# Performance work log

Hardware: AMD Instinct MI355X
Metric: run time of the kernel (lower is better)

The kernel has to match this reference:

```python
import jax, jax.numpy as jnp
import numpy as np

H = 1024          # hidden_size
NH = 16           # num_heads = hidden_size // head_dim
DK = 64           # head_dim (key)
DV = 64           # head_v_dim
VDIM = 1024       # value_dim
DECAY_LR, GATE_LR, A_LR, V_LR = 64, 160, 64, 64
W_SCALE = -0.6065306597126334  # -exp(-0.5)
GN_EPS = 64 * 1e-5             # head_dim * norm_eps


def _lora(x, A, B, b, act):
    h = x @ A.T
    if act is not None:
        h = act(h)
    y = h @ B.T
    return y if b is None else y + b


def setup_inputs() -> dict:
    key = jax.random.key(0)
    ks = iter(jax.random.split(key, 40))
    def n(shape, s=0.02):
        return jax.random.normal(next(ks), shape, dtype=jnp.float32) * s
    inp = {
        'hidden_states': jax.random.normal(next(ks), (8, 2048, H), jnp.float32),
        'v_first': jax.random.normal(next(ks), (8, 2048, VDIM), jnp.float32),
        'x_r': n((1, 1, H), 0.5), 'x_w': n((1, 1, H), 0.5), 'x_k': n((1, 1, H), 0.5),
        'x_v': n((1, 1, H), 0.5), 'x_a': n((1, 1, H), 0.5), 'x_g': n((1, 1, H), 0.5),
        'k_k': 0.71 + n((H,), 0.05),
        'k_a': 1.02 + n((H,), 0.05),
        'r_k': -0.04 + n((NH, DK), 0.05),
        'W_r': n((H, H)), 'W_k': n((H, H)), 'W_v': n((VDIM, H)), 'W_o': n((H, VDIM)),
        'w_lora_A': n((DECAY_LR, H)), 'w_lora_B': n((H, DECAY_LR)), 'w_lora_b': n((H,), 0.5) - 4.0,
        'a_lora_A': n((A_LR, H)), 'a_lora_B': n((H, A_LR)), 'a_lora_b': n((H,), 0.1),
        'v_lora_A': n((V_LR, H)), 'v_lora_B': n((VDIM, V_LR)), 'v_lora_b': 0.73 + n((VDIM,), 0.1),
        'g_lora_A': n((GATE_LR, H)), 'g_lora_B': n((VDIM, GATE_LR)),
        'gn_w': jnp.ones((VDIM,), jnp.float32), 'gn_b': jnp.zeros((VDIM,), jnp.float32),
    }
    return inp


def reference(hidden_states, v_first, x_r, x_w, x_k, x_v, x_a, x_g, k_k, k_a, r_k,
              W_r, W_k, W_v, W_o, w_lora_A, w_lora_B, w_lora_b,
              a_lora_A, a_lora_B, a_lora_b, v_lora_A, v_lora_B, v_lora_b,
              g_lora_A, g_lora_B, gn_w, gn_b):
    x = hidden_states
    B_, T, _ = x.shape
    # token shift: delta[t] = x[t-1] - x[t], x[-1] = 0
    shifted = jnp.pad(x, ((0, 0), (1, 0), (0, 0)))[:, :T]
    delta = shifted - x
    xr = x + delta * x_r; xw = x + delta * x_w; xk = x + delta * x_k
    xv = x + delta * x_v; xa = x + delta * x_a; xg = x + delta * x_g

    r = xr @ W_r.T
    w = W_SCALE * jax.nn.sigmoid(_lora(xw, w_lora_A, w_lora_B, w_lora_b, jnp.tanh))  # log-decay in (-e^-0.5, 0)
    k = xk @ W_k.T
    v = xv @ W_v.T
    v = v + (v_first - v) * jax.nn.sigmoid(_lora(xv, v_lora_A, v_lora_B, v_lora_b, None))  # layer_idx != 0
    a = jax.nn.sigmoid(_lora(xa, a_lora_A, a_lora_B, a_lora_b, None))
    g = _lora(xg, g_lora_A, g_lora_B, None, jax.nn.sigmoid)

    kk = (k * k_k).reshape(B_, T, NH, DK)
    kk = kk / jnp.maximum(jnp.linalg.norm(kk, axis=-1, keepdims=True), 1e-12)  # l2 norm per head
    k = k * (1.0 + (a - 1.0) * k_a)

    rh = r.reshape(B_, T, NH, DK)
    wh = w.reshape(B_, T, NH, DK)
    kh = k.reshape(B_, T, NH, DK)
    vh = v.reshape(B_, T, NH, DV)
    ah = -kk                               # delta-rule 'a' (removal direction)
    bh = kk * a.reshape(B_, T, NH, DK)     # delta-rule 'b' (write direction)

    def step(S, inputs):
        # S: [B, H, DK, DV]; inputs each [B, H, D]
        r_t, w_t, k_t, v_t, a_t, b_t = inputs
        sa = jnp.einsum('bhk,bhkv->bhv', a_t, S)
        S = S * jnp.exp(w_t)[..., None] \
            + jnp.einsum('bhk,bhv->bhkv', b_t, sa) \
            + jnp.einsum('bhk,bhv->bhkv', k_t, v_t)
        o_t = jnp.einsum('bhk,bhkv->bhv', r_t, S)
        return S, o_t

    seq = tuple(jnp.moveaxis(t, 1, 0) for t in (rh, wh, kh, vh, ah, bh))  # [T,B,H,D]
    S0 = jnp.zeros((B_, NH, DK, DV), dtype=x.dtype)
    _, o = jax.lax.scan(step, S0, seq)
    o = jnp.moveaxis(o, 0, 1)  # [B, T, NH, DV]

    # GroupNorm with num_groups = num_heads over value_dim channels == per-head LayerNorm (no per-head affine)
    mu = o.mean(-1, keepdims=True)
    var = o.var(-1, keepdims=True)
    on = ((o - mu) / jnp.sqrt(var + GN_EPS)).reshape(B_, T, VDIM) * gn_w + gn_b

    bonus = ((rh * kh * r_k).sum(-1, keepdims=True) * vh).reshape(B_, T, VDIM)
    out = ((on + bonus) * g) @ W_o.T
    return out
```

## Files before the change

### kernel.cpp

```cpp
#include <hip/hip_runtime.h>
#include <hip/hip_bf16.h>


#define DEVI __device__ __forceinline__

constexpr int TSEQ = 2048;
constexpr int HID  = 1024;
constexpr int BTOT = 16384;
constexpr int CCH  = 32;
constexpr int NCH  = TSEQ / CCH;
constexpr int L4N  = 352;
constexpr float W_SCALE = -0.6065306597126334f;
constexpr float GN_EPS  = 6.4e-4f;

using s16x8  = __attribute__((ext_vector_type(8))) short;
using f32x4v = __attribute__((ext_vector_type(4))) float;

DEVI float4 ld4(const float* p) { return *reinterpret_cast<const float4*>(p); }
DEVI void   st4(float* p, float4 v) { *reinterpret_cast<float4*>(p) = v; }
DEVI float  sigf(float x) { return 1.0f / (1.0f + __expf(-x)); }
DEVI unsigned short bfr(float f) {
    unsigned int u = __float_as_uint(f);
    return (unsigned short)((u + 0x7fffu + ((u >> 16) & 1u)) >> 16);
}
DEVI float bff(unsigned short s) { return __uint_as_float(((unsigned int)s) << 16); }
DEVI unsigned int pk2(float lo, float hi) {
    return ((unsigned int)bfr(hi) << 16) | (unsigned int)bfr(lo);
}
DEVI f32x4v MF(s16x8 a, s16x8 b, f32x4v c) {
    return __builtin_amdgcn_mfma_f32_16x16x32_bf16(a, b, c, 0, 0, 0);
}
DEVI void gl16(const void* g, void* l) {
    __builtin_amdgcn_global_load_lds(
        (const __attribute__((address_space(1))) unsigned int*)g,
        (__attribute__((address_space(3))) unsigned int*)l, 16, 0, 0);
}
DEVI void gl4(const void* g, void* l) {
    __builtin_amdgcn_global_load_lds(
        (const __attribute__((address_space(1))) unsigned int*)g,
        (__attribute__((address_space(3))) unsigned int*)l, 4, 0, 0);
}

__global__ __launch_bounds__(256) void cast_kernel(
        const float* __restrict__ s, unsigned short* __restrict__ d, int n) {
    int i = (blockIdx.x * 256 + threadIdx.x) * 4;
    if (i >= n) return;
    float4 v = ld4(s + i);
    ushort4 o; o.x = bfr(v.x); o.y = bfr(v.y); o.z = bfr(v.z); o.w = bfr(v.w);
    *reinterpret_cast<ushort4*>(d + i) = o;
}

__global__ __launch_bounds__(256) void proj3_kernel(
        const float* __restrict__ x,
        const float* __restrict__ cr, const float* __restrict__ ck,
        const float* __restrict__ cv,
        const unsigned short* __restrict__ Wr, const unsigned short* __restrict__ Wk,
        const unsigned short* __restrict__ Wv,
        unsigned short* __restrict__ Ro, unsigned short* __restrict__ Ko,
        unsigned short* __restrict__ Vo) {
    __shared__ __align__(16) unsigned short As[3][64 * 32];
    __shared__ __align__(16) unsigned short Bs[3][128 * 32];
    const int tid = threadIdx.x;
    const int w = tid >> 6, l = tid & 63;
    const int bm = blockIdx.x * 64, bn = blockIdx.y * 128;
    const int wm = w >> 1, wn = w & 1;
    const int lr = l & 15, lq = l >> 4, lk = lq * 8;

    f32x4v acc[3][2][4];
#pragma unroll
    for (int p = 0; p < 3; p++)
#pragma unroll
        for (int i = 0; i < 2; i++)
#pragma unroll
            for (int j = 0; j < 4; j++)
#pragma unroll
                for (int q = 0; q < 4; q++) acc[p][i][j][q] = 0.f;

    const float* cvs[3] = {cr, ck, cv};
    const unsigned short* Ws[3] = {Wr, Wk, Wv};

    for (int k0 = 0; k0 < HID; k0 += 32) {
        {
            const int row = tid >> 2, kp = (tid & 3) * 8;
            const int gr = bm + row;
            const float* xp = x + (size_t)gr * HID + k0 + kp;
            float4 x0 = ld4(xp), x1 = ld4(xp + 4);
            float4 p0 = make_float4(0.f, 0.f, 0.f, 0.f), p1 = p0;
            if ((gr & (TSEQ - 1)) != 0) { p0 = ld4(xp - HID); p1 = ld4(xp - HID + 4); }
            float xb[8] = {x0.x, x0.y, x0.z, x0.w, x1.x, x1.y, x1.z, x1.w};
            float dx[8] = {p0.x - x0.x, p0.y - x0.y, p0.z - x0.z, p0.w - x0.w,
                           p1.x - x1.x, p1.y - x1.y, p1.z - x1.z, p1.w - x1.w};
#pragma unroll
            for (int p = 0; p < 3; p++) {
                float4 c0 = ld4(cvs[p] + k0 + kp), c1 = ld4(cvs[p] + k0 + kp + 4);
                float cc[8] = {c0.x, c0.y, c0.z, c0.w, c1.x, c1.y, c1.z, c1.w};
                uint4 u;
                u.x = pk2(fmaf(dx[0], cc[0], xb[0]), fmaf(dx[1], cc[1], xb[1]));
                u.y = pk2(fmaf(dx[2], cc[2], xb[2]), fmaf(dx[3], cc[3], xb[3]));
                u.z = pk2(fmaf(dx[4], cc[4], xb[4]), fmaf(dx[5], cc[5], xb[5]));
                u.w = pk2(fmaf(dx[6], cc[6], xb[6]), fmaf(dx[7], cc[7], xb[7]));
                *reinterpret_cast<uint4*>(&As[p][row * 32 + kp]) = u;
            }
        }
#pragma unroll
        for (int p = 0; p < 3; p++)
#pragma unroll
            for (int c = 0; c < 2; c++) {
                int idx = c * 256 + tid;
                int rw = idx >> 2, kp2 = (idx & 3) * 8;
                gl16(Ws[p] + (size_t)(bn + rw) * HID + k0 + kp2,
                     &Bs[p][c * 2048 + w * 512]);
            }
        __syncthreads();
#pragma unroll
        for (int p = 0; p < 3; p++) {
            s16x8 af[2], bf4[4];
#pragma unroll
            for (int i = 0; i < 2; i++)
                af[i] = *reinterpret_cast<const s16x8*>(
                    &As[p][(wm * 32 + i * 16 + lr) * 32 + lk]);
#pragma unroll
            for (int j = 0; j < 4; j++)
                bf4[j] = *reinterpret_cast<const s16x8*>(
                    &Bs[p][(wn * 64 + j * 16 + lr) * 32 + lk]);
#pragma unroll
            for (int i = 0; i < 2; i++)
#pragma unroll
                for (int j = 0; j < 4; j++)
                    acc[p][i][j] = MF(af[i], bf4[j], acc[p][i][j]);
        }
        __syncthreads();
    }

    unsigned short* dsts[3] = {Ro, Ko, Vo};
#pragma unroll
    for (int p = 0; p < 3; p++)
#pragma unroll
        for (int i = 0; i < 2; i++)
#pragma unroll
            for (int j = 0; j < 4; j++)
#pragma unroll
                for (int q = 0; q < 4; q++) {
                    const int grow = bm + wm * 32 + i * 16 + lq * 4 + q;
                    const int gcol = bn + wn * 64 + j * 16 + lr;
                    dsts[p][(size_t)grow * HID + gcol] = bfr(acc[p][i][j][q]);
                }
}

__global__ __launch_bounds__(256) void lora4_kernel(
        const float* __restrict__ x,
        const float* __restrict__ cv_, const float* __restrict__ cw_,
        const float* __restrict__ ca_, const float* __restrict__ cg_,
        const unsigned short* __restrict__ LW, unsigned short* __restrict__ H1) {
    __shared__ __align__(16) unsigned short As[4][64 * 32];
    __shared__ __align__(16) unsigned short Bs[L4N * 32];
    const int tid = threadIdx.x;
    const int w = tid >> 6, l = tid & 63;
    const int lr = l & 15, lq = l >> 4, lk = lq * 8;
    const int bm = blockIdx.x * 64;
    const float* cvs[4] = {cv_, cw_, ca_, cg_};

    f32x4v acc[22];
#pragma unroll
    for (int j = 0; j < 22; j++)
#pragma unroll
        for (int q = 0; q < 4; q++) acc[j][q] = 0.f;

    for (int k0 = 0; k0 < HID; k0 += 32) {
        {
            const int row = tid >> 2, kp = (tid & 3) * 8;
            const int gr = bm + row;
            const float* xp = x + (size_t)gr * HID + k0 + kp;
            float4 x0 = ld4(xp), x1 = ld4(xp + 4);
            float4 p0 = make_float4(0.f, 0.f, 0.f, 0.f), p1 = p0;
            if ((gr & (TSEQ - 1)) != 0) { p0 = ld4(xp - HID); p1 = ld4(xp - HID + 4); }
            float xb[8] = {x0.x, x0.y, x0.z, x0.w, x1.x, x1.y, x1.z, x1.w};
            float dx[8] = {p0.x - x0.x, p0.y - x0.y, p0.z - x0.z, p0.w - x0.w,
                           p1.x - x1.x, p1.y - x1.y, p1.z - x1.z, p1.w - x1.w};
#pragma unroll
            for (int p = 0; p < 4; p++) {
                float4 c0 = ld4(cvs[p] + k0 + kp), c1 = ld4(cvs[p] + k0 + kp + 4);
                float cc[8] = {c0.x, c0.y, c0.z, c0.w, c1.x, c1.y, c1.z, c1.w};
                uint4 u;
                u.x = pk2(fmaf(dx[0], cc[0], xb[0]), fmaf(dx[1], cc[1], xb[1]));
                u.y = pk2(fmaf(dx[2], cc[2], xb[2]), fmaf(dx[3], cc[3], xb[3]));
                u.z = pk2(fmaf(dx[4], cc[4], xb[4]), fmaf(dx[5], cc[5], xb[5]));
                u.w = pk2(fmaf(dx[6], cc[6], xb[6]), fmaf(dx[7], cc[7], xb[7]));
                *reinterpret_cast<uint4*>(&As[p][row * 32 + kp]) = u;
            }
        }
#pragma unroll
        for (int c = 0; c < 6; c++) {
            int idx = c * 256 + tid;
            if (idx < L4N * 4) {
                gl16(LW + (size_t)(idx >> 2) * HID + (idx & 3) * 8 + k0,
                     (char*)&Bs[0] + (c * 256 + w * 64) * 16);
            }
        }
        __syncthreads();
        s16x8 af[4];
#pragma unroll
        for (int p = 0; p < 4; p++)
            af[p] = *reinterpret_cast<const s16x8*>(&As[p][(w * 16 + lr) * 32 + lk]);
#pragma unroll
        for (int j = 0; j < 22; j++) {
            const int grp = (j < 4) ? 0 : (j < 8) ? 1 : (j < 12) ? 2 : 3;
            s16x8 bf = *reinterpret_cast<const s16x8*>(&Bs[(j * 16 + lr) * 32 + lk]);
            acc[j] = MF(af[grp], bf, acc[j]);
        }
        __syncthreads();
    }

#pragma unroll
    for (int j = 0; j < 22; j++)
#pragma unroll
        for (int q = 0; q < 4; q++) {
            const int grow = bm + w * 16 + lq * 4 + q;
            const int gcol = j * 16 + lr;
            float d = acc[j][q];
            if (j >= 4 && j < 8) d = tanhf(d);
            else if (j >= 12) d = sigf(d);
            H1[(size_t)grow * L4N + gcol] = bfr(d);
        }
}

template<int BM, int BN, int MODE, bool OUTBF>
__global__ __launch_bounds__(256) void mgemm(
        const unsigned short* __restrict__ Ab, const unsigned short* __restrict__ Bw,
        void* Cout, int N, int K, int lda,
        const float* __restrict__ bias,
        const unsigned short* aux1, const float* __restrict__ aux2) {
    constexpr int BK = 32;
    constexpr int WM_ = (BN == 128) ? 2 : 4;
    constexpr int WN_ = (BN == 128) ? 2 : 1;
    constexpr int WTM = BM / WM_, WTN = BN / WN_;
    constexpr int MF_ = WTM / 16, NF = WTN / 16;
    constexpr int ACALLS = (BM * BK) / 2048;
    constexpr int BCALLS = (BN * BK) / 2048;
    __shared__ __align__(16) unsigned short As[BM * BK];
    __shared__ __align__(16) unsigned short Bs[BN * BK];
    const int tid = threadIdx.x;
    const int w = tid >> 6, l = tid & 63;
    const int bm = blockIdx.x * BM, bn = blockIdx.y * BN;
    const int wm = w / WN_, wn = w % WN_;
    const int lr = l & 15, lk = (l >> 4) * 8;

    f32x4v acc[MF_][NF];
#pragma unroll
    for (int i = 0; i < MF_; i++)
#pragma unroll
        for (int j = 0; j < NF; j++)
#pragma unroll
            for (int q = 0; q < 4; q++) acc[i][j][q] = 0.f;

    for (int k0 = 0; k0 < K; k0 += BK) {
#pragma unroll
        for (int c = 0; c < ACALLS; c++) {
            int idx = c * 256 + tid;
            int row = idx >> 2, kp = (idx & 3) * 8;
            gl16(Ab + (size_t)(bm + row) * lda + k0 + kp, &As[c * 2048 + w * 512]);
        }
#pragma unroll
        for (int c = 0; c < BCALLS; c++) {
            int idx = c * 256 + tid;
            int row = idx >> 2, kp = (idx & 3) * 8;
            int gc = bn + row; if (gc > N - 1) gc = N - 1;
            gl16(Bw + (size_t)gc * K + k0 + kp, &Bs[c * 2048 + w * 512]);
        }
        __syncthreads();
        s16x8 afx[MF_], bfx[NF];
#pragma unroll
        for (int i = 0; i < MF_; i++)
            afx[i] = *reinterpret_cast<const s16x8*>(&As[(wm * WTM + i * 16 + lr) * BK + lk]);
#pragma unroll
        for (int j = 0; j < NF; j++)
            bfx[j] = *reinterpret_cast<const s16x8*>(&Bs[(wn * WTN + j * 16 + lr) * BK + lk]);
#pragma unroll
        for (int i = 0; i < MF_; i++)
#pragma unroll
            for (int j = 0; j < NF; j++)
                acc[i][j] = __builtin_amdgcn_mfma_f32_16x16x32_bf16(
                    afx[i], bfx[j], acc[i][j], 0, 0, 0);
        __syncthreads();
    }

#pragma unroll
    for (int i = 0; i < MF_; i++) {
        const int grow0 = bm + wm * WTM + i * 16 + (l >> 4) * 4;
#pragma unroll
        for (int j = 0; j < NF; j++) {
            const int gcol = bn + wn * WTN + j * 16 + lr;
            if (gcol >= N) continue;
            const float bsv = (MODE >= 4) ? bias[gcol] : 0.f;
#pragma unroll
            for (int q = 0; q < 4; q++) {
                const int grow = grow0 + q;
                float d = acc[i][j][q];
                if (MODE == 4) d = sigf(d + bsv);
                else if (MODE == 5) {
                    float v0 = bff(aux1[(size_t)grow * N + gcol]);
                    d = fmaf(aux2[(size_t)grow * N + gcol] - v0, sigf(d + bsv), v0);
                }
                else if (MODE == 6) d = W_SCALE * sigf(d + bsv);
                if (OUTBF) ((unsigned short*)Cout)[(size_t)grow * N + gcol] = bfr(d);
                else       ((float*)Cout)[(size_t)grow * N + gcol] = d;
            }
        }
    }
}

__global__ __launch_bounds__(64) void cprep_kernel(
        unsigned short* __restrict__ K16, unsigned short* __restrict__ A16,
        unsigned short* __restrict__ R16, unsigned short* __restrict__ KK16,
        const unsigned short* __restrict__ W16,
        const float* __restrict__ kkc, const float* __restrict__ kac,
        const float* __restrict__ rkw,
        float* __restrict__ SB, float* __restrict__ Ed,
        unsigned short* __restrict__ MvH, unsigned short* __restrict__ MvL) {
    __shared__ __align__(16) unsigned short sA[32][64], sB[32][64];
    __shared__ __align__(16) float Mab[32][36];
    const int bid = blockIdx.x;
    const int bh = bid >> 6, ch = bid & 63;
    const int bb = bh >> 4, hh = bh & 15;
    const int l = threadIdx.x;
    const int chn = hh * 64 + l;
    const float kkcv = kkc[chn], kacv = kac[chn], rkv = rkw[chn];
    size_t off = ((size_t)(bb * TSEQ) + ch * CCH) * HID + chn;
    float cw = 0.f, er = 1.f;
    for (int i = 0; i < CCH; i++, off += HID) {
        const float k = bff(K16[off]);
        const float a = bff(A16[off]);
        const float r = bff(R16[off]);
        const float wv = bff(W16[off]);
        const float kr = k * kkcv;
        float ss = kr * kr;
        ss += __shfl_xor(ss, 1);  ss += __shfl_xor(ss, 2);
        ss += __shfl_xor(ss, 4);  ss += __shfl_xor(ss, 8);
        ss += __shfl_xor(ss, 16); ss += __shfl_xor(ss, 32);
        const float inv = 1.0f / fmaxf(sqrtf(ss), 1e-12f);
        const float kk = kr * inv;
        const float b  = kk * a;
        const float kn = k * fmaf(a - 1.0f, kacv, 1.0f);
        float s3 = r * kn * rkv;
        s3 += __shfl_xor(s3, 1);  s3 += __shfl_xor(s3, 2);
        s3 += __shfl_xor(s3, 4);  s3 += __shfl_xor(s3, 8);
        s3 += __shfl_xor(s3, 16); s3 += __shfl_xor(s3, 32);
        if (l == 0) SB[(size_t)bh * TSEQ + ch * CCH + i] = s3;
        const float cwp = cw; cw += wv;
        const float ea = __expf(cwp), ei = __expf(-cw);
        er = __expf(cw);
        const unsigned short At = bfr(-kk * ea);
        const unsigned short Bt = bfr(b * ei);
        KK16[off] = At;
        A16[off]  = Bt;
        K16[off]  = bfr(kn * ei);
        R16[off]  = bfr(r * er);
        sA[i][l] = At; sB[i][l] = Bt;
    }
    Ed[((size_t)bh * NCH + ch) * 64 + l] = er;
    __syncthreads();
    const int lr = l & 15, lq = l >> 4;
    f32x4v z4; z4[0] = z4[1] = z4[2] = z4[3] = 0.f;
#pragma unroll
    for (int mi = 0; mi < 2; mi++)
#pragma unroll
        for (int ni = 0; ni < 2; ni++) {
            s16x8 a0 = *reinterpret_cast<const s16x8*>(&sA[mi * 16 + lr][lq * 8]);
            s16x8 a1 = *reinterpret_cast<const s16x8*>(&sA[mi * 16 + lr][32 + lq * 8]);
            s16x8 b0 = *reinterpret_cast<const s16x8*>(&sB[ni * 16 + lr][lq * 8]);
            s16x8 b1 = *reinterpret_cast<const s16x8*>(&sB[ni * 16 + lr][32 + lq * 8]);
            f32x4v m = MF(a1, b1, MF(a0, b0, z4));
#pragma unroll
            for (int q = 0; q < 4; q++) {
                int r = mi * 16 + lq * 4 + q, cc2 = ni * 16 + lr;
                Mab[r][cc2] = (cc2 < r) ? m[q] : 0.f;
            }
        }
    __syncthreads();
    const int j = l & 31;
    float m[32];
#pragma unroll
    for (int i = 0; i < 32; i++) m[i] = (i == j) ? 1.f : 0.f;
#pragma unroll
    for (int i = 1; i < 32; i++) {
        float p0 = 0.f, p1 = 0.f, p2 = 0.f, p3 = 0.f;
#pragma unroll
        for (int k4_ = 0; k4_ < 32; k4_ += 4) {
            if (k4_ >= i) break;
            float4 L4 = *reinterpret_cast<const float4*>(&Mab[i][k4_]);
            p0 = fmaf(L4.x, m[k4_ + 0], p0);
            if (k4_ + 1 < i) p1 = fmaf(L4.y, m[k4_ + 1], p1);
            if (k4_ + 2 < i) p2 = fmaf(L4.z, m[k4_ + 2], p2);
            if (k4_ + 3 < i) p3 = fmaf(L4.w, m[k4_ + 3], p3);
        }
        m[i] += (p0 + p1) + (p2 + p3);
    }
    if (l < 32) {
        unsigned short* dH = MvH + (size_t)(bh * NCH + ch) * 1024;
        unsigned short* dL = MvL + (size_t)(bh * NCH + ch) * 1024;
#pragma unroll
        for (int i = 0; i < 32; i++) {
            unsigned short h = bfr(m[i]);
            dH[i * 32 + j] = h;
            dL[i * 32 + j] = bfr(m[i] - bff(h));
        }
    }
}

__global__ __launch_bounds__(256) void recchunk_kernel(
        const unsigned short* __restrict__ AtG, const unsigned short* __restrict__ BtG,
        const unsigned short* __restrict__ KtG, const unsigned short* __restrict__ RtG,
        const unsigned short* __restrict__ V16, const float* __restrict__ Ed,
        const unsigned short* __restrict__ MvH, const unsigned short* __restrict__ MvL,
        float* __restrict__ Ob) {
    __shared__ __align__(16) unsigned short stT[2][4][CCH][64];
    __shared__ __align__(16) unsigned short stMh[2][32][32], stMl[2][32][32];
    __shared__ __align__(16) unsigned short stV[2][CCH][16];
    __shared__ __align__(16) float stEd[2][64];
    __shared__ __align__(16) unsigned short Shi[16][74], Slo[16][74];
    __shared__ __align__(16) unsigned short BtT[64][42], KtT[64][42];
    __shared__ __align__(16) unsigned short VT[16][42];
    __shared__ __align__(16) unsigned short MakH[32][42], MakL[32][42];
    __shared__ __align__(16) unsigned short MrkH[32][42], MrkL[32][42];
    __shared__ __align__(16) unsigned short MrbH[32][42], MrbL[32][42];
    __shared__ __align__(16) unsigned short rhTH[16][42], rhTL[16][42];

    const int bid = blockIdx.x;
    const int vq = bid >> 7, bh = bid & 127;
    const int tid = threadIdx.x;
    const int w = tid >> 6, l = tid & 63;
    const int lr = l & 15, lq = l >> 4;
    const int bb = bh >> 4, hh = bh & 15;
    const size_t rowoff = ((size_t)bb * TSEQ) * HID + hh * 64;
    const int mi = w >> 1, ni = w & 1;

    const int r8 = l >> 3, ck = l & 7;
    const int swz8 = (ck ^ r8) * 8;

    auto STAGE = [&](int buf, int cn) {
        if (cn >= NCH) return;
        const size_t cb = rowoff + (size_t)(cn * CCH) * HID;
        const unsigned short* srcs[4] = {AtG, BtG, KtG, RtG};
        const unsigned short* T = srcs[w];
#pragma unroll
        for (int c = 0; c < 4; c++)
            gl16(T + cb + (size_t)(c * 8 + r8) * HID + swz8, &stT[buf][w][c * 8][0]);
        if (w == 0) {
            gl16(V16 + cb + (size_t)(l >> 1) * HID + vq * 16 + (l & 1) * 8,
                 &stV[buf][0][0]);
            gl4(Ed + ((size_t)bh * NCH + cn) * 64 + l, &stEd[buf][0]);
        } else if (w == 1) {
#pragma unroll
            for (int c = 0; c < 2; c++)
                gl16(MvH + (size_t)(bh * NCH + cn) * 1024 + c * 512 + l * 8,
                     (char*)&stMh[buf][0][0] + c * 1024);
        } else if (w == 2) {
#pragma unroll
            for (int c = 0; c < 2; c++)
                gl16(MvL + (size_t)(bh * NCH + cn) * 1024 + c * 512 + l * 8,
                     (char*)&stMl[buf][0][0] + c * 1024);
        }
    };

    for (int idx = tid; idx < 16 * 74; idx += 256) {
        ((unsigned short*)Shi)[idx] = 0;
        ((unsigned short*)Slo)[idx] = 0;
    }
    STAGE(0, 0);
    asm volatile("s_waitcnt vmcnt(0)" ::: "memory");
    __syncthreads();

    auto fragT = [&](int bf, int tn, int rbase, int kb) -> s16x8 {
        int row = rbase + lr;
        int chv = ((kb >> 3) + lq) ^ (row & 7);
        return *reinterpret_cast<const s16x8*>(
            (const char*)&stT[bf][tn][0][0] + row * 128 + chv * 16);
    };
    auto fragS = [&](const unsigned short (*Sx)[74], int kb) -> s16x8 {
        return *reinterpret_cast<const s16x8*>(&Sx[lr][kb + lq * 8]);
    };
    auto frag42 = [&](const unsigned short (*T)[42], int rbase) -> s16x8 {
        return *reinterpret_cast<const s16x8*>(&T[rbase + lr][lq * 8]);
    };

    f32x4v Sacc;
#pragma unroll
    for (int q = 0; q < 4; q++) Sacc[q] = 0.f;
    f32x4v z4; z4[0] = z4[1] = z4[2] = z4[3] = 0.f;

    int buf = 0;
    for (int c = 0; c < NCH; c++) {
        STAGE(buf ^ 1, c + 1);
        {
            const int tt = tid & 31, g8 = tid >> 5;
            const int ch = g8 ^ (tt & 7);
            uint4 bu = *reinterpret_cast<const uint4*>(&stT[buf][1][tt][ch * 8]);
            uint4 ku = *reinterpret_cast<const uint4*>(&stT[buf][2][tt][ch * 8]);
            unsigned int bw[4] = {bu.x, bu.y, bu.z, bu.w};
            unsigned int kw[4] = {ku.x, ku.y, ku.z, ku.w};
#pragma unroll
            for (int e = 0; e < 4; e++) {
                BtT[g8 * 8 + 2 * e][tt]     = (unsigned short)(bw[e] & 0xffffu);
                BtT[g8 * 8 + 2 * e + 1][tt] = (unsigned short)(bw[e] >> 16);
                KtT[g8 * 8 + 2 * e][tt]     = (unsigned short)(kw[e] & 0xffffu);
                KtT[g8 * 8 + 2 * e + 1][tt] = (unsigned short)(kw[e] >> 16);
            }
            if (g8 < 4) {
                ushort4 vu = *reinterpret_cast<const ushort4*>(&stV[buf][tt][g8 * 4]);
                VT[g8 * 4 + 0][tt] = vu.x; VT[g8 * 4 + 1][tt] = vu.y;
                VT[g8 * 4 + 2][tt] = vu.z; VT[g8 * 4 + 3][tt] = vu.w;
            }
        }
        s16x8 atm0 = fragT(buf, 0, mi * 16, 0), atm1 = fragT(buf, 0, mi * 16, 32);
        s16x8 rt0  = fragT(buf, 3, mi * 16, 0), rt1  = fragT(buf, 3, mi * 16, 32);
        s16x8 bt0  = fragT(buf, 1, ni * 16, 0), bt1  = fragT(buf, 1, ni * 16, 32);
        s16x8 kt0  = fragT(buf, 2, ni * 16, 0), kt1  = fragT(buf, 2, ni * 16, 32);
        f32x4v mak = MF(atm1, kt1, MF(atm0, kt0, z4));
        f32x4v mrk = MF(rt1, kt1, MF(rt0, kt0, z4));
        f32x4v mrb = MF(rt1, bt1, MF(rt0, bt0, z4));
        f32x4v oac = z4, rhT = z4;
        {
            s16x8 sh0 = fragS(Shi, 0), sh1 = fragS(Shi, 32);
            s16x8 sl0 = fragS(Slo, 0), sl1 = fragS(Slo, 32);
            if (ni == 0) {
                oac = MF(rt1, sl1, MF(rt0, sl0, MF(rt1, sh1, MF(rt0, sh0, z4))));
            } else {
                rhT = MF(sl1, atm1, MF(sl0, atm0, MF(sh1, atm1, MF(sh0, atm0, z4))));
            }
        }
#pragma unroll
        for (int q = 0; q < 4; q++) {
            const int r = mi * 16 + lq * 4 + q, cc = ni * 16 + lr;
            float vv = (cc < r) ? mak[q] : 0.f;
            unsigned short h = bfr(vv);
            MakH[r][cc] = h; MakL[r][cc] = bfr(vv - bff(h));
            vv = (cc <= r) ? mrk[q] : 0.f; h = bfr(vv);
            MrkH[r][cc] = h; MrkL[r][cc] = bfr(vv - bff(h));
            vv = (cc <= r) ? mrb[q] : 0.f; h = bfr(vv);
            MrbH[r][cc] = h; MrbL[r][cc] = bfr(vv - bff(h));
        }
        __syncthreads();
        {
            s16x8 vt0 = frag42(VT, 0);
            if (ni == 0) {
                oac = MF(frag42(MrkL, mi * 16), vt0,
                         MF(frag42(MrkH, mi * 16), vt0, oac));
            } else {
                rhT = MF(vt0, frag42(MakL, mi * 16),
                         MF(vt0, frag42(MakH, mi * 16), rhT));
#pragma unroll
                for (int q = 0; q < 4; q++) {
                    const int r = lq * 4 + q, cc = mi * 16 + lr;
                    unsigned short h = bfr(rhT[q]);
                    rhTH[r][cc] = h; rhTL[r][cc] = bfr(rhT[q] - bff(h));
                }
            }
        }
        __syncthreads();
        if (ni == 1) {
            s16x8 rh0 = frag42(rhTH, 0), rl0 = frag42(rhTL, 0);
            s16x8 mvh = *reinterpret_cast<const s16x8*>(&stMh[buf][mi * 16 + lr][lq * 8]);
            s16x8 mvl = *reinterpret_cast<const s16x8*>(&stMl[buf][mi * 16 + lr][lq * 8]);
            f32x4v sat = MF(rl0, mvh, MF(rh0, mvl, MF(rh0, mvh, z4)));
#pragma unroll
            for (int q = 0; q < 4; q++) {
                const int r = lq * 4 + q, cc = mi * 16 + lr;
                unsigned short h = bfr(sat[q]);
                MakH[r][cc] = h;
                MakL[r][cc] = bfr(sat[q] - bff(h));
            }
        }
        __syncthreads();
        {
            s16x8 sath = frag42(MakH, 0), satl = frag42(MakL, 0);
            if (ni == 0) {
                s16x8 rbh = frag42(MrbH, mi * 16), rbl = frag42(MrbL, mi * 16);
                oac = MF(rbl, sath, MF(rbh, satl, MF(rbh, sath, oac)));
#pragma unroll
                for (int q = 0; q < 4; q++) {
                    const int t = c * CCH + mi * 16 + lq * 4 + q;
                    Ob[rowoff + (size_t)t * HID + vq * 16 + lr] = oac[q];
                }
            }
            s16x8 btf = frag42(BtT, w * 16);
            s16x8 ktf = frag42(KtT, w * 16);
            s16x8 vta = frag42(VT, 0);
            const float ed = stEd[buf][w * 16 + lr];
            Sacc = MF(sath, btf, Sacc);
            Sacc = MF(satl, btf, Sacc);
            Sacc = MF(vta, ktf, Sacc);
#pragma unroll
            for (int q = 0; q < 4; q++) {
                Sacc[q] *= ed;
                unsigned short h = bfr(Sacc[q]);
                Shi[lq * 4 + q][w * 16 + lr] = h;
                Slo[lq * 4 + q][w * 16 + lr] = bfr(Sacc[q] - bff(h));
            }
        }
        asm volatile("s_waitcnt vmcnt(0)" ::: "memory");
        __syncthreads();
        buf ^= 1;
    }
}

__global__ __launch_bounds__(256) void post_kernel(
        const float* __restrict__ Ob, const unsigned short* __restrict__ V16,
        const unsigned short* __restrict__ G16, const float* __restrict__ SB,
        const float* __restrict__ gnw, const float* __restrict__ gnb,
        unsigned short* __restrict__ Y16) {
    const int row = blockIdx.x;
    const int tid = threadIdx.x;
    const int c   = tid * 4;
    const size_t off = (size_t)row * HID + c;
    float4 o4 = ld4(Ob + off);
    ushort4 vu = *reinterpret_cast<const ushort4*>(V16 + off);
    ushort4 gu = *reinterpret_cast<const ushort4*>(G16 + off);
    float v[4] = {bff(vu.x), bff(vu.y), bff(vu.z), bff(vu.w)};
    float g[4] = {bff(gu.x), bff(gu.y), bff(gu.z), bff(gu.w)};
    const int hh = tid >> 4;
    const int bb = row >> 11, t = row & (TSEQ - 1);
    const float s3 = SB[((size_t)(bb * 16 + hh)) * TSEQ + t];

    float s1 = o4.x + o4.y + o4.z + o4.w;
    float s2 = o4.x*o4.x + o4.y*o4.y + o4.z*o4.z + o4.w*o4.w;
#pragma unroll
    for (int m = 1; m < 16; m <<= 1) {
        s1 += __shfl_xor(s1, m); s2 += __shfl_xor(s2, m);
    }
    const float mu  = s1 * (1.0f / 64.0f);
    const float var = s2 * (1.0f / 64.0f) - mu * mu;
    const float inv = rsqrtf(var + GN_EPS);
    float4 gw = ld4(gnw + c), gb = ld4(gnb + c);
    ushort4 y;
    y.x = bfr((fmaf((o4.x - mu) * inv, gw.x, gb.x) + s3 * v[0]) * g[0]);
    y.y = bfr((fmaf((o4.y - mu) * inv, gw.y, gb.y) + s3 * v[1]) * g[1]);
    y.z = bfr((fmaf((o4.z - mu) * inv, gw.z, gb.z) + s3 * v[2]) * g[2]);
    y.w = bfr((fmaf((o4.w - mu) * inv, gw.w, gb.w) + s3 * v[3]) * g[3]);
    *reinterpret_cast<ushort4*>(Y16 + off) = y;
}

extern "C" void kernel_launch(void* const* d_in, const int* in_sizes, int n_in,
                              void* d_out, int out_size, void* d_ws, size_t ws_size,
                              hipStream_t stream) {
    const float* x   = (const float*)d_in[0];
    const float* vf  = (const float*)d_in[1];
    const float* x_r = (const float*)d_in[2];
    const float* x_w = (const float*)d_in[3];
    const float* x_k = (const float*)d_in[4];
    const float* x_v = (const float*)d_in[5];
    const float* x_a = (const float*)d_in[6];
    const float* x_g = (const float*)d_in[7];
    const float* k_k = (const float*)d_in[8];
    const float* k_a = (const float*)d_in[9];
    const float* r_k = (const float*)d_in[10];
    const float* W_r = (const float*)d_in[11];
    const float* W_k = (const float*)d_in[12];
    const float* W_v = (const float*)d_in[13];
    const float* W_o = (const float*)d_in[14];
    const float* wA  = (const float*)d_in[15];
    const float* wB  = (const float*)d_in[16];
    const float* wb  = (const float*)d_in[17];
    const float* aA  = (const float*)d_in[18];
    const float* aB  = (const float*)d_in[19];
    const float* ab  = (const float*)d_in[20];
    const float* vA  = (const float*)d_in[21];
    const float* vB  = (const float*)d_in[22];
    const float* vb  = (const float*)d_in[23];
    const float* gA  = (const float*)d_in[24];
    const float* gB  = (const float*)d_in[25];
    const float* gnw = (const float*)d_in[26];
    const float* gnb = (const float*)d_in[27];
    float* out = (float*)d_out;

    float* ws = (float*)d_ws;
    const size_t SZ = (size_t)BTOT * HID;
    const size_t HH = (size_t)HID * HID;
    float*          REG  = ws;
    unsigned short* P    = (unsigned short*)(ws + SZ);
    unsigned short* R16  = P;
    unsigned short* K16  = P + 1 * SZ;
    unsigned short* V16  = P + 2 * SZ;
    unsigned short* A16  = P + 3 * SZ;
    unsigned short* KK16 = P + 4 * SZ;
    unsigned short* H1   = P + 5 * SZ;
    unsigned short* WR   = H1 + (size_t)BTOT * L4N;
    unsigned short* Wr16 = WR;
    unsigned short* Wk16 = WR + 1 * HH;
    unsigned short* Wv16 = WR + 2 * HH;
    unsigned short* Wo16 = WR + 3 * HH;
    unsigned short* LW   = WR + 4 * HH;
    unsigned short* vB16 = LW + (size_t)L4N * HID;
    unsigned short* wB16 = vB16 + 65536;
    unsigned short* aB16 = wB16 + 65536;
    unsigned short* gB16 = aB16 + 65536;
    float*          SB   = (float*)(gB16 + 163840);
    float*          Ed   = SB + (size_t)128 * TSEQ;
    unsigned short* W16   = (unsigned short*)REG;
    unsigned short* MinvH = (unsigned short*)(REG + 8 * 1024 * 1024);
    unsigned short* MinvL = MinvH + (size_t)128 * NCH * 1024;
    unsigned short* Y16  = R16;
    unsigned short* G16  = (unsigned short*)REG;

    const dim3 blk(256);
    const dim3 gBig(128, 8);
    const dim3 gP3(BTOT / 64, 8);
    const unsigned short* nu = nullptr;
    const float* np = nullptr;

    auto CAST = [&](const float* s, unsigned short* d, int n) {
        cast_kernel<<<dim3((n / 4 + 255) / 256), blk, 0, stream>>>(s, d, n);
    };
    CAST(W_r, Wr16, (int)HH); CAST(W_k, Wk16, (int)HH);
    CAST(W_v, Wv16, (int)HH); CAST(W_o, Wo16, (int)HH);
    CAST(vA, LW + 0 * 65536, 65536);
    CAST(wA, LW + 1 * 65536, 65536);
    CAST(aA, LW + 2 * 65536, 65536);
    CAST(gA, LW + 3 * 65536, 163840);
    CAST(vB, vB16, 65536); CAST(wB, wB16, 65536);
    CAST(aB, aB16, 65536); CAST(gB, gB16, 163840);

    proj3_kernel<<<gP3, blk, 0, stream>>>(
        x, x_r, x_k, x_v, Wr16, Wk16, Wv16, R16, K16, V16);
    lora4_kernel<<<dim3(BTOT / 64), blk, 0, stream>>>(
        x, x_v, x_w, x_a, x_g, LW, H1);
    mgemm<128,128,5,true><<<gBig, blk, 0, stream>>>(
        H1 + 0, vB16, V16, HID, 64, L4N, vb, V16, vf);
    mgemm<128,128,6,true><<<gBig, blk, 0, stream>>>(
        H1 + 64, wB16, W16, HID, 64, L4N, wb, nu, np);
    mgemm<128,128,4,true><<<gBig, blk, 0, stream>>>(
        H1 + 128, aB16, A16, HID, 64, L4N, ab, nu, np);
    cprep_kernel<<<dim3(128 * NCH), dim3(64), 0, stream>>>(
        K16, A16, R16, KK16, W16, k_k, k_a, r_k, SB, Ed, MinvH, MinvL);
    recchunk_kernel<<<dim3(512), blk, 0, stream>>>(
        KK16, A16, K16, R16, V16, Ed, MinvH, MinvL, out);
    mgemm<128,128,0,true><<<gBig, blk, 0, stream>>>(
        H1 + 192, gB16, G16, HID, 160, L4N, np, nu, np);
    post_kernel<<<dim3(BTOT), blk, 0, stream>>>(
        out, V16, G16, SB, gnw, gnb, Y16);
    mgemm<128,128,0,false><<<gBig, blk, 0, stream>>>(
        Y16, Wo16, out, HID, HID, HID, np, nu, np);
    (void)in_sizes; (void)n_in; (void)out_size; (void)ws_size;
}
```

Before: 1.051 ms.

## Batch weight casts, merge LoRA-B GEMMs, fuse GroupNorm/gate into Wo GEMM prologue

```diff
diff --git a/kernel.cpp b/kernel.cpp
--- a/kernel.cpp
+++ b/kernel.cpp
@@ -27,6 +27,12 @@
 DEVI unsigned int pk2(float lo, float hi) {
     return ((unsigned int)bfr(hi) << 16) | (unsigned int)bfr(lo);
 }
+DEVI void up8(uint4 u, float* f) {
+    f[0]=bff((unsigned short)(u.x & 0xffffu)); f[1]=bff((unsigned short)(u.x >> 16));
+    f[2]=bff((unsigned short)(u.y & 0xffffu)); f[3]=bff((unsigned short)(u.y >> 16));
+    f[4]=bff((unsigned short)(u.z & 0xffffu)); f[5]=bff((unsigned short)(u.z >> 16));
+    f[6]=bff((unsigned short)(u.w & 0xffffu)); f[7]=bff((unsigned short)(u.w >> 16));
+}
 DEVI f32x4v MF(s16x8 a, s16x8 b, f32x4v c) {
     return __builtin_amdgcn_mfma_f32_16x16x32_bf16(a, b, c, 0, 0, 0);
 }
@@ -41,13 +47,21 @@
         (__attribute__((address_space(3))) unsigned int*)l, 4, 0, 0);
 }
 
-__global__ __launch_bounds__(256) void cast_kernel(
-        const float* __restrict__ s, unsigned short* __restrict__ d, int n) {
-    int i = (blockIdx.x * 256 + threadIdx.x) * 4;
-    if (i >= n) return;
-    float4 v = ld4(s + i);
+struct CastArgs {
+    const float* src[12];
+    unsigned short* dst[12];
+    int start4[13];
+};
+__global__ __launch_bounds__(256) void cast_all_kernel(CastArgs a) {
+    int i4 = blockIdx.x * 256 + threadIdx.x;
+    if (i4 >= a.start4[12]) return;
+    int seg = 0;
+#pragma unroll
+    for (int s = 1; s < 12; s++) seg += (i4 >= a.start4[s]) ? 1 : 0;
+    int off = (i4 - a.start4[seg]) * 4;
+    float4 v = ld4(a.src[seg] + off);
     ushort4 o; o.x = bfr(v.x); o.y = bfr(v.y); o.z = bfr(v.z); o.w = bfr(v.w);
-    *reinterpret_cast<ushort4*>(d + i) = o;
+    *reinterpret_cast<ushort4*>(a.dst[seg] + off) = o;
 }
 
 __global__ __launch_bounds__(256) void proj3_kernel(
@@ -222,6 +236,91 @@
             else if (j >= 12) d = sigf(d);
             H1[(size_t)grow * L4N + gcol] = bfr(d);
         }
+}
+
+__global__ __launch_bounds__(256) void stage2_kernel(
+        const unsigned short* __restrict__ H1,
+        const unsigned short* __restrict__ vB16, const unsigned short* __restrict__ wB16,
+        const unsigned short* __restrict__ aB16,
+        const float* __restrict__ vb, const float* __restrict__ wb,
+        const float* __restrict__ ab,
+        unsigned short* __restrict__ Vout, unsigned short* __restrict__ Wout,
+        unsigned short* __restrict__ Aout,
+        const unsigned short* __restrict__ aux1, const float* __restrict__ aux2) {
+    const int z = blockIdx.z;
+    const unsigned short* Bw = (z == 0) ? vB16 : (z == 1) ? wB16 : aB16;
+    const float* bias = (z == 0) ? vb : (z == 1) ? wb : ab;
+    unsigned short* Cout = (z == 0) ? Vout : (z == 1) ? Wout : Aout;
+    const int aoff = z * 64;
+    __shared__ __align__(16) unsigned short As[128 * 32];
+    __shared__ __align__(16) unsigned short Bs[128 * 32];
+    const int tid = threadIdx.x;
+    const int w = tid >> 6, l = tid & 63;
+    const int bm = blockIdx.x * 128, bn = blockIdx.y * 128;
+    const int wm = w >> 1, wn = w & 1;
+    const int lr = l & 15, lk = (l >> 4) * 8;
+
+    f32x4v acc[4][4];
+#pragma unroll
+    for (int i = 0; i < 4; i++)
+#pragma unroll
+        for (int j = 0; j < 4; j++)
+#pragma unroll
+            for (int q = 0; q < 4; q++) acc[i][j][q] = 0.f;
+
+    for (int k0 = 0; k0 < 64; k0 += 32) {
+#pragma unroll
+        for (int c = 0; c < 2; c++) {
+            int idx = c * 256 + tid;
+            int row = idx >> 2, kp = (idx & 3) * 8;
+            gl16(H1 + (size_t)(bm + row) * L4N + aoff + k0 + kp,
+                 &As[c * 2048 + w * 512]);
+        }
+#pragma unroll
+        for (int c = 0; c < 2; c++) {
+            int idx = c * 256 + tid;
+            int row = idx >> 2, kp = (idx & 3) * 8;
+            gl16(Bw + (size_t)(bn + row) * 64 + k0 + kp, &Bs[c * 2048 + w * 512]);
+        }
+        __syncthreads();
+        s16x8 afx[4], bfx[4];
+#pragma unroll
+        for (int i = 0; i < 4; i++)
+            afx[i] = *reinterpret_cast<const s16x8*>(&As[(wm * 64 + i * 16 + lr) * 32 + lk]);
+#pragma unroll
+        for (int j = 0; j < 4; j++)
+            bfx[j] = *reinterpret_cast<const s16x8*>(&Bs[(wn * 64 + j * 16 + lr) * 32 + lk]);
+#pragma unroll
+        for (int i = 0; i < 4; i++)
+#pragma unroll
+            for (int j = 0; j < 4; j++)
+                acc[i][j] = MF(afx[i], bfx[j], acc[i][j]);
+        __syncthreads();
+    }
+
+#pragma unroll
+    for (int i = 0; i < 4; i++) {
+        const int grow0 = bm + wm * 64 + i * 16 + (l >> 4) * 4;
+#pragma unroll
+        for (int j = 0; j < 4; j++) {
+            const int gcol = bn + wn * 64 + j * 16 + lr;
+            const float bsv = bias[gcol];
+#pragma unroll
+            for (int q = 0; q < 4; q++) {
+                const int grow = grow0 + q;
+                float d = acc[i][j][q];
+                if (z == 0) {
+                    float v0 = bff(aux1[(size_t)grow * HID + gcol]);
+                    d = fmaf(aux2[(size_t)grow * HID + gcol] - v0, sigf(d + bsv), v0);
+                } else if (z == 1) {
+                    d = W_SCALE * sigf(d + bsv);
+                } else {
+                    d = sigf(d + bsv);
+                }
+                Cout[(size_t)grow * HID + gcol] = bfr(d);
+            }
+        }
+    }
 }
 
 template<int BM, int BN, int MODE, bool OUTBF>
@@ -291,17 +390,10 @@
         for (int j = 0; j < NF; j++) {
             const int gcol = bn + wn * WTN + j * 16 + lr;
             if (gcol >= N) continue;
-            const float bsv = (MODE >= 4) ? bias[gcol] : 0.f;
 #pragma unroll
             for (int q = 0; q < 4; q++) {
                 const int grow = grow0 + q;
                 float d = acc[i][j][q];
-                if (MODE == 4) d = sigf(d + bsv);
-                else if (MODE == 5) {
-                    float v0 = bff(aux1[(size_t)grow * N + gcol]);
-                    d = fmaf(aux2[(size_t)grow * N + gcol] - v0, sigf(d + bsv), v0);
-                }
-                else if (MODE == 6) d = W_SCALE * sigf(d + bsv);
                 if (OUTBF) ((unsigned short*)Cout)[(size_t)grow * N + gcol] = bfr(d);
                 else       ((float*)Cout)[(size_t)grow * N + gcol] = d;
             }
@@ -412,7 +504,7 @@
         const unsigned short* __restrict__ KtG, const unsigned short* __restrict__ RtG,
         const unsigned short* __restrict__ V16, const float* __restrict__ Ed,
         const unsigned short* __restrict__ MvH, const unsigned short* __restrict__ MvL,
-        float* __restrict__ Ob) {
+        unsigned short* __restrict__ Ob16) {
     __shared__ __align__(16) unsigned short stT[2][4][CCH][64];
     __shared__ __align__(16) unsigned short stMh[2][32][32], stMl[2][32][32];
     __shared__ __align__(16) unsigned short stV[2][CCH][16];
@@ -579,7 +671,7 @@
 #pragma unroll
                 for (int q = 0; q < 4; q++) {
                     const int t = c * CCH + mi * 16 + lq * 4 + q;
-                    Ob[rowoff + (size_t)t * HID + vq * 16 + lr] = oac[q];
+                    Ob16[rowoff + (size_t)t * HID + vq * 16 + lr] = bfr(oac[q]);
                 }
             }
             s16x8 btf = frag42(BtT, w * 16);
@@ -603,40 +695,111 @@
     }
 }
 
-__global__ __launch_bounds__(256) void post_kernel(
-        const float* __restrict__ Ob, const unsigned short* __restrict__ V16,
-        const unsigned short* __restrict__ G16, const float* __restrict__ SB,
-        const float* __restrict__ gnw, const float* __restrict__ gnb,
-        unsigned short* __restrict__ Y16) {
+__global__ __launch_bounds__(256) void stats_kernel(
+        const unsigned short* __restrict__ O16, float* __restrict__ MS) {
     const int row = blockIdx.x;
     const int tid = threadIdx.x;
-    const int c   = tid * 4;
-    const size_t off = (size_t)row * HID + c;
-    float4 o4 = ld4(Ob + off);
-    ushort4 vu = *reinterpret_cast<const ushort4*>(V16 + off);
-    ushort4 gu = *reinterpret_cast<const ushort4*>(G16 + off);
-    float v[4] = {bff(vu.x), bff(vu.y), bff(vu.z), bff(vu.w)};
-    float g[4] = {bff(gu.x), bff(gu.y), bff(gu.z), bff(gu.w)};
-    const int hh = tid >> 4;
-    const int bb = row >> 11, t = row & (TSEQ - 1);
-    const float s3 = SB[((size_t)(bb * 16 + hh)) * TSEQ + t];
-
-    float s1 = o4.x + o4.y + o4.z + o4.w;
-    float s2 = o4.x*o4.x + o4.y*o4.y + o4.z*o4.z + o4.w*o4.w;
+    const int c = tid * 4;
+    ushort4 ou = *reinterpret_cast<const ushort4*>(O16 + (size_t)row * HID + c);
+    float o[4] = {bff(ou.x), bff(ou.y), bff(ou.z), bff(ou.w)};
+    float s1 = o[0] + o[1] + o[2] + o[3];
+    float s2 = o[0]*o[0] + o[1]*o[1] + o[2]*o[2] + o[3]*o[3];
 #pragma unroll
     for (int m = 1; m < 16; m <<= 1) {
         s1 += __shfl_xor(s1, m); s2 += __shfl_xor(s2, m);
     }
-    const float mu  = s1 * (1.0f / 64.0f);
-    const float var = s2 * (1.0f / 64.0f) - mu * mu;
-    const float inv = rsqrtf(var + GN_EPS);
-    float4 gw = ld4(gnw + c), gb = ld4(gnb + c);
-    ushort4 y;
-    y.x = bfr((fmaf((o4.x - mu) * inv, gw.x, gb.x) + s3 * v[0]) * g[0]);
-    y.y = bfr((fmaf((o4.y - mu) * inv, gw.y, gb.y) + s3 * v[1]) * g[1]);
-    y.z = bfr((fmaf((o4.z - mu) * inv, gw.z, gb.z) + s3 * v[2]) * g[2]);
-    y.w = bfr((fmaf((o4.w - mu) * inv, gw.w, gb.w) + s3 * v[3]) * g[3]);
-    *reinterpret_cast<ushort4*>(Y16 + off) = y;
+    if ((tid & 15) == 0) {
+        const int hh = tid >> 4;
+        const float mu = s1 * (1.0f / 64.0f);
+        const float var = s2 * (1.0f / 64.0f) - mu * mu;
+        float2 v; v.x = mu; v.y = rsqrtf(var + GN_EPS);
+        *reinterpret_cast<float2*>(MS + (size_t)row * 32 + hh * 2) = v;
+    }
+}
+
+__global__ __launch_bounds__(256) void wogemm_kernel(
+        const unsigned short* __restrict__ O16, const unsigned short* __restrict__ V16,
+        const unsigned short* __restrict__ G16, const float* __restrict__ SB,
+        const float* __restrict__ MS, const float* __restrict__ gnw,
+        const float* __restrict__ gnb, const unsigned short* __restrict__ Wo,
+        float* __restrict__ out) {
+    __shared__ __align__(16) unsigned short As[128 * 32];
+    __shared__ __align__(16) unsigned short Bs[128 * 32];
+    const int tid = threadIdx.x;
+    const int w = tid >> 6, l = tid & 63;
+    const int bm = blockIdx.x * 128, bn = blockIdx.y * 128;
+    const int wm = w >> 1, wn = w & 1;
+    const int lr = l & 15, lk = (l >> 4) * 8;
+
+    f32x4v acc[4][4];
+#pragma unroll
+    for (int i = 0; i < 4; i++)
+#pragma unroll
+        for (int j = 0; j < 4; j++)
+#pragma unroll
+            for (int q = 0; q < 4; q++) acc[i][j][q] = 0.f;
+
+    for (int k0 = 0; k0 < HID; k0 += 32) {
+#pragma unroll
+        for (int c = 0; c < 2; c++) {
+            int idx = c * 256 + tid;
+            int row = idx >> 2, kp = (idx & 3) * 8;
+            const int gr = bm + row;
+            const size_t rb = (size_t)gr * HID + k0 + kp;
+            uint4 ou = *reinterpret_cast<const uint4*>(O16 + rb);
+            uint4 vu = *reinterpret_cast<const uint4*>(V16 + rb);
+            uint4 gu = *reinterpret_cast<const uint4*>(G16 + rb);
+            float o8[8], v8[8], g8[8];
+            up8(ou, o8); up8(vu, v8); up8(gu, g8);
+            const int hh = (k0 + kp) >> 6;
+            float2 ms = *reinterpret_cast<const float2*>(MS + (size_t)gr * 32 + hh * 2);
+            const float s3 = SB[((size_t)(gr >> 11) * 16 + hh) * TSEQ + (gr & (TSEQ - 1))];
+            float4 w0 = ld4(gnw + k0 + kp), w1 = ld4(gnw + k0 + kp + 4);
+            float4 b0 = ld4(gnb + k0 + kp), b1 = ld4(gnb + k0 + kp + 4);
+            float wn8[8] = {w0.x, w0.y, w0.z, w0.w, w1.x, w1.y, w1.z, w1.w};
+            float bn8[8] = {b0.x, b0.y, b0.z, b0.w, b1.x, b1.y, b1.z, b1.w};
+            float y[8];
+#pragma unroll
+            for (int e = 0; e < 8; e++)
+                y[e] = (fmaf((o8[e] - ms.x) * ms.y, wn8[e], bn8[e]) + s3 * v8[e]) * g8[e];
+            uint4 u;
+            u.x = pk2(y[0], y[1]); u.y = pk2(y[2], y[3]);
+            u.z = pk2(y[4], y[5]); u.w = pk2(y[6], y[7]);
+            *reinterpret_cast<uint4*>(&As[idx * 8]) = u;
+        }
+#pragma unroll
+        for (int c = 0; c < 2; c++) {
+            int idx = c * 256 + tid;
+            int row = idx >> 2, kp = (idx & 3) * 8;
+            gl16(Wo + (size_t)(bn + row) * HID + k0 + kp, &Bs[c * 2048 + w * 512]);
+        }
+        __syncthreads();
+        s16x8 afx[4], bfx[4];
+#pragma unroll
+        for (int i = 0; i < 4; i++)
+            afx[i] = *reinterpret_cast<const s16x8*>(&As[(wm * 64 + i * 16 + lr) * 32 + lk]);
+#pragma unroll
+        for (int j = 0; j < 4; j++)
+            bfx[j] = *reinterpret_cast<const s16x8*>(&Bs[(wn * 64 + j * 16 + lr) * 32 + lk]);
+#pragma unroll
+        for (int i = 0; i < 4; i++)
+#pragma unroll
+            for (int j = 0; j < 4; j++)
+                acc[i][j] = MF(afx[i], bfx[j], acc[i][j]);
+        __syncthreads();
+    }
+
+#pragma unroll
+    for (int i = 0; i < 4; i++) {
+        const int grow0 = bm + wm * 64 + i * 16 + (l >> 4) * 4;
+#pragma unroll
+        for (int j = 0; j < 4; j++) {
+            const int gcol = bn + wn * 64 + j * 16 + lr;
+#pragma unroll
+            for (int q = 0; q < 4; q++)
+                out[(size_t)(grow0 + q) * HID + gcol] = acc[i][j][q];
+        }
+    }
 }
 
 extern "C" void kernel_launch(void* const* d_in, const int* in_sizes, int n_in,
@@ -695,11 +858,12 @@
     unsigned short* gB16 = aB16 + 65536;
     float*          SB   = (float*)(gB16 + 163840);
     float*          Ed   = SB + (size_t)128 * TSEQ;
+    float*          MS   = Ed;
     unsigned short* W16   = (unsigned short*)REG;
+    unsigned short* O16   = (unsigned short*)REG;
     unsigned short* MinvH = (unsigned short*)(REG + 8 * 1024 * 1024);
     unsigned short* MinvL = MinvH + (size_t)128 * NCH * 1024;
-    unsigned short* Y16  = R16;
-    unsigned short* G16  = (unsigned short*)REG;
+    unsigned short* G16   = (unsigned short*)(REG + 8 * 1024 * 1024);
 
     const dim3 blk(256);
     const dim3 gBig(128, 8);
@@ -707,37 +871,36 @@
     const unsigned short* nu = nullptr;
     const float* np = nullptr;
 
-    auto CAST = [&](const float* s, unsigned short* d, int n) {
-        cast_kernel<<<dim3((n / 4 + 255) / 256), blk, 0, stream>>>(s, d, n);
-    };
-    CAST(W_r, Wr16, (int)HH); CAST(W_k, Wk16, (int)HH);
-    CAST(W_v, Wv16, (int)HH); CAST(W_o, Wo16, (int)HH);
-    CAST(vA, LW + 0 * 65536, 65536);
-    CAST(wA, LW + 1 * 65536, 65536);
-    CAST(aA, LW + 2 * 65536, 65536);
-    CAST(gA, LW + 3 * 65536, 163840);
-    CAST(vB, vB16, 65536); CAST(wB, wB16, 65536);
-    CAST(aB, aB16, 65536); CAST(gB, gB16, 163840);
+    CastArgs ca;
+    const float* srcs[12] = {W_r, W_k, W_v, W_o, vA, wA, aA, gA, vB, wB, aB, gB};
+    unsigned short* dsts[12] = {Wr16, Wk16, Wv16, Wo16,
+                                LW, LW + 65536, LW + 131072, LW + 196608,
+                                vB16, wB16, aB16, gB16};
+    int cnts[12] = {(int)HH, (int)HH, (int)HH, (int)HH,
+                    65536, 65536, 65536, 163840, 65536, 65536, 65536, 163840};
+    int acc4 = 0;
+    for (int s = 0; s < 12; s++) {
+        ca.src[s] = srcs[s]; ca.dst[s] = dsts[s];
+        ca.start4[s] = acc4;
+        acc4 += cnts[s] / 4;
+    }
+    ca.start4[12] = acc4;
+    cast_all_kernel<<<dim3((acc4 + 255) / 256), blk, 0, stream>>>(ca);
 
     proj3_kernel<<<gP3, blk, 0, stream>>>(
         x, x_r, x_k, x_v, Wr16, Wk16, Wv16, R16, K16, V16);
     lora4_kernel<<<dim3(BTOT / 64), blk, 0, stream>>>(
         x, x_v, x_w, x_a, x_g, LW, H1);
-    mgemm<128,128,5,true><<<gBig, blk, 0, stream>>>(
-        H1 + 0, vB16, V16, HID, 64, L4N, vb, V16, vf);
-    mgemm<128,128,6,true><<<gBig, blk, 0, stream>>>(
-        H1 + 64, wB16, W16, HID, 64, L4N, wb, nu, np);
-    mgemm<128,128,4,true><<<gBig, blk, 0, stream>>>(
-        H1 + 128, aB16, A16, HID, 64, L4N, ab, nu, np);
+    stage2_kernel<<<dim3(128, 8, 3), blk, 0, stream>>>(
+        H1, vB16, wB16, aB16, vb, wb, ab, V16, W16, A16, V16, vf);
     cprep_kernel<<<dim3(128 * NCH), dim3(64), 0, stream>>>(
         K16, A16, R16, KK16, W16, k_k, k_a, r_k, SB, Ed, MinvH, MinvL);
     recchunk_kernel<<<dim3(512), blk, 0, stream>>>(
-        KK16, A16, K16, R16, V16, Ed, MinvH, MinvL, out);
+        KK16, A16, K16, R16, V16, Ed, MinvH, MinvL, O16);
     mgemm<128,128,0,true><<<gBig, blk, 0, stream>>>(
         H1 + 192, gB16, G16, HID, 160, L4N, np, nu, np);
-    post_kernel<<<dim3(BTOT), blk, 0, stream>>>(
-        out, V16, G16, SB, gnw, gnb, Y16);
-    mgemm<128,128,0,false><<<gBig, blk, 0, stream>>>(
-        Y16, Wo16, out, HID, HID, HID, np, nu, np);
+    stats_kernel<<<dim3(BTOT), blk, 0, stream>>>(O16, MS);
+    wogemm_kernel<<<gBig, blk, 0, stream>>>(
+        O16, V16, G16, SB, MS, gnw, gnb, Wo16, out);
     (void)in_sizes; (void)n_in; (void)out_size; (void)ws_size;
 }
```

Result: no change. 1.045 ms (-0.6%).
